# Kernel tuning notes

Hardware: AMD Instinct MI355X
Metric: run time of the kernel (lower is better)

The kernel has to match this reference:

```python
import jax, jax.numpy as jnp
import numpy as np

B, L, E, S, V = 256, 64, 128, 16, 50000
H0, H1 = 16 * E, 4 * E  # dense hidden sizes from dense_sequence_lengths [64,16,4]
PAD_IDX, UNK_IDX = 1, 0


def setup_inputs() -> dict:
    key = jax.random.key(0)
    ks = jax.random.split(key, 12)
    text_lengths = jax.random.randint(ks[0], (B,), 1, L + 1)
    text_lengths = text_lengths.at[0].set(L)  # ensure max(lengths) == L
    raw_tokens = jax.random.randint(ks[1], (B, L), 2, V)
    pos = jnp.arange(L)
    text_batch = jnp.where(pos[None, :] < text_lengths[:, None], raw_tokens, PAD_IDX)
    sentiment_ids = jax.random.randint(ks[2], (B,), 0, 2)

    emb_table = jax.random.normal(ks[3], (V, E), dtype=jnp.float32) * 0.1
    emb_table = emb_table.at[UNK_IDX].set(0.0).at[PAD_IDX].set(0.0)
    sentiment_table = jax.random.normal(ks[4], (2, S), dtype=jnp.float32)
    sentiment_table = sentiment_table / jnp.linalg.norm(sentiment_table, axis=1, keepdims=True)

    D_in = L * E + S + E  # 8336
    W0 = jax.random.normal(ks[5], (D_in, H0), dtype=jnp.float32) * 0.02
    b0 = jax.random.normal(ks[6], (H0,), dtype=jnp.float32) * 0.02
    W1 = jax.random.normal(ks[7], (H0, H1), dtype=jnp.float32) * 0.02
    b1 = jax.random.normal(ks[8], (H1,), dtype=jnp.float32) * 0.02
    Wp = jax.random.normal(ks[9], (H1, 1), dtype=jnp.float32) * 0.02
    bp = jax.random.normal(ks[10], (1,), dtype=jnp.float32) * 0.02
    return {"text_batch": text_batch, "text_lengths": text_lengths,
            "sentiment_ids": sentiment_ids, "emb_table": emb_table,
            "sentiment_table": sentiment_table, "W0": W0, "b0": b0,
            "W1": W1, "b1": b1, "Wp": Wp, "bp": bp}


def reference(text_batch, text_lengths, sentiment_ids, emb_table, sentiment_table,
              W0, b0, W1, b1, Wp, bp):
    # nn.Embedding(max_norm=1.0): renorm rows with norm > 1 (torch uses eps 1e-7)
    norms = jnp.linalg.norm(emb_table, axis=1, keepdims=True)
    w = emb_table * jnp.where(norms > 1.0, 1.0 / (norms + 1e-7), 1.0)
    emb = w[text_batch]                       # (B, L, E)  (dropout is identity in eval)
    sent_flat = emb.reshape(B, L * E)         # flattened sentence embedding
    sv = sentiment_table[sentiment_ids]       # (B, S)

    # First dense layer on concat([sent_flat, sv, word_emb]) factored so the
    # shared sentence/sentiment part is computed once per sentence.
    W_sent, W_snt, W_word = W0[:L * E], W0[L * E:L * E + S], W0[L * E + S:]
    base = sent_flat @ W_sent + sv @ W_snt + b0            # (B, H0)
    h0 = jax.nn.relu(base[:, None, :] + jnp.einsum('ble,eh->blh', emb, W_word))  # (B, L, H0)
    h1 = jax.nn.relu(jnp.einsum('blh,hk->blk', h0, W1) + b1)                      # (B, L, H1)

    # Positions >= text_length keep their zero initialization in encoded_batch
    mask = jnp.arange(L)[None, :] < text_lengths[:, None]  # (B, L)
    enc = jnp.where(mask[:, :, None], h1, 0.0)

    pred = jax.nn.sigmoid(enc @ Wp + bp)[..., 0]           # (B, L)
    return pred
```

## Files before the change

### kernel.cpp

```cpp
#include <hip/hip_runtime.h>
#include <hip/hip_bf16.h>

#define B_   256
#define L_   64
#define E_   128
#define S_   16
#define H0_  2048
#define H1_  512
#define LE_  8192
#define DIN_ 8336
#define NROW 16384

typedef __attribute__((ext_vector_type(8))) short short8_t;
typedef __attribute__((ext_vector_type(4))) float f32x4;

static __device__ __forceinline__ f32x4 mfma16(short8_t a, short8_t b, f32x4 c){
  return __builtin_amdgcn_mfma_f32_16x16x32_bf16(a, b, c, 0, 0, 0);
}

static __device__ __forceinline__ unsigned short f2bf(float x){
  unsigned u = __builtin_bit_cast(unsigned, x);
  unsigned r = u + 0x7FFFu + ((u >> 16) & 1u);
  return (unsigned short)(r >> 16);
}

static __device__ __forceinline__ void gl_lds16(const void* g, void* l){
  __builtin_amdgcn_global_load_lds((const __attribute__((address_space(1))) unsigned*)g,
                                   (__attribute__((address_space(3))) unsigned*)l, 16, 0, 0);
}

__global__ __launch_bounds__(256) void k_scan(const int* __restrict__ lens,
    int* __restrict__ rowmap, int* __restrict__ offs, int* __restrict__ meta){
  __shared__ int sh[256];
  int t = threadIdx.x;
  int v = lens[t];
  sh[t] = v;
  __syncthreads();
  for (int d = 1; d < 256; d <<= 1){
    int y = (t >= d) ? sh[t - d] : 0;
    __syncthreads();
    sh[t] += y;
    __syncthreads();
  }
  int off = sh[t] - v;
  int nv = sh[255];
  offs[t] = off;
  if (t == 0){
    meta[0] = nv;
    meta[1] = (nv + 63) & ~63;
    meta[2] = (nv + 127) & ~127;
  }
  for (int l = 0; l < v; ++l) rowmap[off + l] = t * 64 + l;
  for (int i = nv + t; i < NROW; i += 256) rowmap[i] = 0;
}

__global__ __launch_bounds__(256) void k_transpose_cvt(const float* __restrict__ src,
    unsigned short* __restrict__ dst, int R, int C){
  __shared__ unsigned short tile[64][65];
  int R0 = blockIdx.x * 64, C0 = blockIdx.y * 64;
  int t = threadIdx.x;
  int row = t >> 2, c16 = (t & 3) * 16;
  int gr = R0 + row;
  if (gr < R){
    const float* p = src + (size_t)gr * C + C0 + c16;
    #pragma unroll
    for (int j = 0; j < 16; j += 4){
      float4 v = *reinterpret_cast<const float4*>(p + j);
      tile[row][c16+j+0] = f2bf(v.x);
      tile[row][c16+j+1] = f2bf(v.y);
      tile[row][c16+j+2] = f2bf(v.z);
      tile[row][c16+j+3] = f2bf(v.w);
    }
  }
  __syncthreads();
  int orow = t >> 2, r16 = (t & 3) * 16;
  unsigned short buf[16];
  #pragma unroll
  for (int j = 0; j < 16; ++j) buf[j] = tile[r16 + j][orow];
  unsigned short* q = dst + (size_t)(C0 + orow) * R + R0 + r16;
  if (R0 + r16 + 15 < R){
    *reinterpret_cast<short8_t*>(q)     = *reinterpret_cast<short8_t*>(&buf[0]);
    *reinterpret_cast<short8_t*>(q + 8) = *reinterpret_cast<short8_t*>(&buf[8]);
  } else {
    for (int j = 0; j < 16; ++j) if (R0 + r16 + j < R) q[j] = buf[j];
  }
}

__global__ __launch_bounds__(256) void k_gather(const int* __restrict__ tokens,
    const float* __restrict__ emb, unsigned short* __restrict__ ebf){
  int wid  = blockIdx.x * 4 + (threadIdx.x >> 6);
  int lane = threadIdx.x & 63;
  int tok  = tokens[wid];
  const float* row = emb + (size_t)tok * E_;
  float2 v = *reinterpret_cast<const float2*>(row + lane * 2);
  float ss = v.x * v.x + v.y * v.y;
  #pragma unroll
  for (int m = 1; m < 64; m <<= 1) ss += __shfl_xor(ss, m, 64);
  float nrm = sqrtf(ss);
  float scale = (nrm > 1.0f) ? 1.0f / (nrm + 1e-7f) : 1.0f;
  unsigned a = f2bf(v.x * scale), b = f2bf(v.y * scale);
  *reinterpret_cast<unsigned*>(ebf + (size_t)wid * E_ + lane * 2) = a | (b << 16);
}

static __device__ __forceinline__ void stage64(
    const unsigned short* __restrict__ Asrc, size_t strideA, int m0,
    const unsigned short* __restrict__ Bsrc, size_t strideB, int n0,
    int kbA, int kbB, int w, int lane,
    unsigned short* Al, unsigned short* Bl){
  int rsub = lane >> 3;
  int csw  = 8 * ((lane & 7) ^ rsub);
  #pragma unroll
  for (int c = 0; c < 2; ++c){
    int q = w * 2 + c;
    gl_lds16(Asrc + (size_t)(m0 + q*8 + rsub) * strideA + kbA + csw, Al + q * 512);
  }
  #pragma unroll
  for (int c = 0; c < 4; ++c){
    int q = w * 4 + c;
    gl_lds16(Bsrc + (size_t)(n0 + q*8 + rsub) * strideB + kbB + csw, Bl + q * 512);
  }
}

__global__ __launch_bounds__(256, 2) void k_gemmA(const unsigned short* __restrict__ ebf,
    const unsigned short* __restrict__ W0T, float* __restrict__ part){
  __shared__ unsigned short Al[2][64*64];
  __shared__ unsigned short Bl[2][128*64];
  int bid = blockIdx.x;
  int mt = bid & 3, nt = (bid >> 2) & 15, kw = bid >> 6;
  int m0 = mt * 64, n0 = nt * 128, k0 = kw * 2048;
  int t = threadIdx.x, lane = t & 63, w = t >> 6;
  int wm = w >> 1, wn = w & 1;
  int sw = (lane & 7) * 8, hi = (lane >> 4) * 8, fr = lane & 15;
  f32x4 acc[2][4];
  #pragma unroll
  for (int m = 0; m < 2; ++m)
    #pragma unroll
    for (int n = 0; n < 4; ++n) acc[m][n] = (f32x4){0.f,0.f,0.f,0.f};

  stage64(ebf, LE_, m0, W0T, DIN_, n0, k0, k0, w, lane, Al[0], Bl[0]);
  __syncthreads();
  for (int it = 0; it < 32; ++it){
    int cur = it & 1;
    if (it + 1 < 32)
      stage64(ebf, LE_, m0, W0T, DIN_, n0, k0 + (it+1)*64, k0 + (it+1)*64,
              w, lane, Al[cur^1], Bl[cur^1]);
    #pragma unroll
    for (int ks = 0; ks < 2; ++ks){
      int col = (ks*32 + hi) ^ sw;
      short8_t af[2], bfr[4];
      #pragma unroll
      for (int m = 0; m < 2; ++m)
        af[m] = *reinterpret_cast<const short8_t*>(&Al[cur][(wm*32 + m*16 + fr)*64 + col]);
      #pragma unroll
      for (int n = 0; n < 4; ++n)
        bfr[n] = *reinterpret_cast<const short8_t*>(&Bl[cur][(wn*64 + n*16 + fr)*64 + col]);
      #pragma unroll
      for (int m = 0; m < 2; ++m)
        #pragma unroll
        for (int n = 0; n < 4; ++n) acc[m][n] = mfma16(af[m], bfr[n], acc[m][n]);
    }
    __syncthreads();
  }
  float* P = part + (size_t)kw * B_ * H0_;
  #pragma unroll
  for (int m = 0; m < 2; ++m)
    #pragma unroll
    for (int n = 0; n < 4; ++n)
      #pragma unroll
      for (int i = 0; i < 4; ++i){
        int r = m0 + wm*32 + m*16 + (lane >> 4)*4 + i;
        int c = n0 + wn*64 + n*16 + fr;
        P[(size_t)r * H0_ + c] = acc[m][n][i];
      }
}

__global__ __launch_bounds__(256) void k_base(const int* __restrict__ sid,
    const float* __restrict__ stab, const float* __restrict__ W0,
    const float* __restrict__ b0, const float* __restrict__ part,
    float* __restrict__ base){
  int idx = blockIdx.x * 256 + threadIdx.x;
  int b = idx >> 11, h = idx & 2047;
  const float* sv = stab + sid[b] * S_;
  float acc = b0[h];
  #pragma unroll
  for (int s = 0; s < S_; ++s) acc += sv[s] * W0[(size_t)(LE_ + s) * H0_ + h];
  #pragma unroll
  for (int kw = 0; kw < 4; ++kw) acc += part[(size_t)kw * B_ * H0_ + idx];
  base[idx] = acc;
}

__global__ __launch_bounds__(256, 2) void k_h0(const unsigned short* __restrict__ ebf,
    const unsigned short* __restrict__ W0T, const float* __restrict__ base,
    const int* __restrict__ rowmap, const int* __restrict__ meta,
    unsigned short* __restrict__ h0c){
  int m0 = blockIdx.x * 128;
  if (m0 >= meta[2]) return;
  int n0 = blockIdx.y * 128;
  __shared__ char smem[65536];
  unsigned short* Alds = (unsigned short*)smem;
  unsigned short* Blds = (unsigned short*)(smem + 32768);
  int t = threadIdx.x, lane = t & 63, w = t >> 6;
  int wm = w >> 1, wn = w & 1;
  int sw = (lane & 7) * 8, hi = (lane >> 4) * 8, fr = lane & 15;

  {
    int rsub = lane >> 4;
    int bc = lane & 15;
    #pragma unroll
    for (int c = 0; c < 8; ++c){
      int q = w * 8 + c;
      int row7 = (q & 1) * 4 + rsub;
      int csw = 8 * (bc ^ row7);
      int rm = rowmap[m0 + q*4 + rsub];
      gl_lds16(ebf + (size_t)rm * E_ + csw, Alds + q * 512);
    }
    #pragma unroll
    for (int c = 0; c < 8; ++c){
      int q = w * 8 + c;
      int row7 = (q & 1) * 4 + rsub;
      int csw = 8 * (bc ^ row7);
      gl_lds16(W0T + (size_t)(n0 + q*4 + rsub) * DIN_ + (LE_ + S_) + csw, Blds + q * 512);
    }
  }
  __syncthreads();

  f32x4 acc[4][4];
  #pragma unroll
  for (int m = 0; m < 4; ++m)
    #pragma unroll
    for (int n = 0; n < 4; ++n) acc[m][n] = (f32x4){0.f,0.f,0.f,0.f};
  #pragma unroll
  for (int ks = 0; ks < 4; ++ks){
    int col = (ks*32 + hi) ^ sw;
    short8_t af[4], bfr[4];
    #pragma unroll
    for (int m = 0; m < 4; ++m)
      af[m] = *reinterpret_cast<const short8_t*>(&Alds[(wm*64 + m*16 + fr)*128 + col]);
    #pragma unroll
    for (int n = 0; n < 4; ++n)
      bfr[n] = *reinterpret_cast<const short8_t*>(&Blds[(wn*64 + n*16 + fr)*128 + col]);
    #pragma unroll
    for (int m = 0; m < 4; ++m)
      #pragma unroll
      for (int n = 0; n < 4; ++n) acc[m][n] = mfma16(af[m], bfr[n], acc[m][n]);
  }
  __syncthreads();
  unsigned short* Hs = (unsigned short*)smem;
  #pragma unroll
  for (int m = 0; m < 4; ++m)
    #pragma unroll
    for (int i = 0; i < 4; ++i){
      int row_l = wm*64 + m*16 + (lane >> 4)*4 + i;
      int rm = rowmap[m0 + row_l];
      const float* bb = base + (size_t)(rm >> 6) * H0_ + n0;
      #pragma unroll
      for (int n = 0; n < 4; ++n){
        int col_l = wn*64 + n*16 + fr;
        float vv = acc[m][n][i] + bb[col_l];
        Hs[row_l * 136 + col_l] = f2bf(vv > 0.f ? vv : 0.f);
      }
    }
  __syncthreads();
  int row = t >> 1, half = t & 1;
  const unsigned short* hp = Hs + row * 136 + half * 64;
  unsigned short* gp = h0c + (size_t)(m0 + row) * H0_ + n0 + half * 64;
  #pragma unroll
  for (int j = 0; j < 8; ++j)
    *reinterpret_cast<short8_t*>(gp + j * 8) = *reinterpret_cast<const short8_t*>(hp + j * 8);
}

__global__ __launch_bounds__(256, 2) void k_h1(const unsigned short* __restrict__ h0c,
    const unsigned short* __restrict__ W1T, const float* __restrict__ b1,
    const float* __restrict__ Wp, const int* __restrict__ meta,
    float* __restrict__ logitc){
  int m0 = blockIdx.x * 64;
  if (m0 >= meta[1]) return;
  int n0 = blockIdx.y * 128;
  __shared__ unsigned short Al[2][64*64];
  __shared__ unsigned short Bl[2][128*64];
  int t = threadIdx.x, lane = t & 63, w = t >> 6;
  int wm = w >> 1, wn = w & 1;
  int sw = (lane & 7) * 8, hi = (lane >> 4) * 8, fr = lane & 15;
  f32x4 acc[2][4];
  #pragma unroll
  for (int m = 0; m < 2; ++m)
    #pragma unroll
    for (int n = 0; n < 4; ++n) acc[m][n] = (f32x4){0.f,0.f,0.f,0.f};

  stage64(h0c, H0_, m0, W1T, H0_, n0, 0, 0, w, lane, Al[0], Bl[0]);
  __syncthreads();
  for (int it = 0; it < 32; ++it){
    int cur = it & 1;
    if (it + 1 < 32)
      stage64(h0c, H0_, m0, W1T, H0_, n0, (it+1)*64, (it+1)*64, w, lane, Al[cur^1], Bl[cur^1]);
    #pragma unroll
    for (int ks = 0; ks < 2; ++ks){
      int col = (ks*32 + hi) ^ sw;
      short8_t af[2], bfr[4];
      #pragma unroll
      for (int m = 0; m < 2; ++m)
        af[m] = *reinterpret_cast<const short8_t*>(&Al[cur][(wm*32 + m*16 + fr)*64 + col]);
      #pragma unroll
      for (int n = 0; n < 4; ++n)
        bfr[n] = *reinterpret_cast<const short8_t*>(&Bl[cur][(wn*64 + n*16 + fr)*64 + col]);
      #pragma unroll
      for (int m = 0; m < 2; ++m)
        #pragma unroll
        for (int n = 0; n < 4; ++n) acc[m][n] = mfma16(af[m], bfr[n], acc[m][n]);
    }
    __syncthreads();
  }
  float b1v[4], wpv[4];
  #pragma unroll
  for (int n = 0; n < 4; ++n){
    int col = n0 + wn*64 + n*16 + fr;
    b1v[n] = b1[col]; wpv[n] = Wp[col];
  }
  #pragma unroll
  for (int m = 0; m < 2; ++m)
    #pragma unroll
    for (int i = 0; i < 4; ++i){
      float p = 0.f;
      #pragma unroll
      for (int n = 0; n < 4; ++n){
        float h = acc[m][n][i] + b1v[n];
        h = h > 0.f ? h : 0.f;
        p += h * wpv[n];
      }
      p += __shfl_xor(p, 1); p += __shfl_xor(p, 2);
      p += __shfl_xor(p, 4); p += __shfl_xor(p, 8);
      if ((lane & 15) == 0)
        atomicAdd(&logitc[m0 + wm*32 + m*16 + (lane >> 4)*4 + i], p);
    }
}

__global__ __launch_bounds__(256) void k_finish(const int* __restrict__ lens,
    const int* __restrict__ offs, const float* __restrict__ logitc,
    const float* __restrict__ bp, float* __restrict__ out){
  int idx = blockIdx.x * 256 + threadIdx.x;
  int b = idx >> 6, l = idx & 63;
  float x = bp[0];
  if (l < lens[b]) x += logitc[offs[b] + l];
  out[idx] = 1.f / (1.f + expf(-x));
}

extern "C" void kernel_launch(void* const* d_in, const int* in_sizes, int n_in,
                              void* d_out, int out_size, void* d_ws, size_t ws_size,
                              hipStream_t stream){
  const int*   text = (const int*)d_in[0];
  const int*   lens = (const int*)d_in[1];
  const int*   sid  = (const int*)d_in[2];
  const float* emb  = (const float*)d_in[3];
  const float* stab = (const float*)d_in[4];
  const float* W0   = (const float*)d_in[5];
  const float* b0   = (const float*)d_in[6];
  const float* W1   = (const float*)d_in[7];
  const float* b1   = (const float*)d_in[8];
  const float* Wp   = (const float*)d_in[9];
  const float* bp   = (const float*)d_in[10];
  float* out = (float*)d_out;

  char* ws = (char*)d_ws;
  unsigned short* ebf    = (unsigned short*)(ws);
  unsigned short* W0T    = (unsigned short*)(ws + 4194304);
  unsigned short* W1T    = (unsigned short*)(ws + 38338560);
  float*          base   = (float*)(ws + 40435712);
  float*          part   = (float*)(ws + 42532864);
  float*          logitc = (float*)(ws + 50921472);
  int*            rowmap = (int*)(ws + 50987008);
  int*            offs   = (int*)(ws + 51052544);
  int*            meta   = (int*)(ws + 51053568);
  unsigned short* h0c    = (unsigned short*)(ws + 51054592);

  hipMemsetAsync(logitc, 0, NROW * 4, stream);
  hipLaunchKernelGGL(k_scan,      dim3(1),        dim3(256), 0, stream, lens, rowmap, offs, meta);
  hipLaunchKernelGGL(k_gather,    dim3(4096),     dim3(256), 0, stream, text, emb, ebf);
  hipLaunchKernelGGL(k_transpose_cvt, dim3(131, 32), dim3(256), 0, stream, W0, W0T, DIN_, H0_);
  hipLaunchKernelGGL(k_transpose_cvt, dim3(32, 8),   dim3(256), 0, stream, W1, W1T, H0_, H1_);
  hipLaunchKernelGGL(k_gemmA,     dim3(256),      dim3(256), 0, stream, ebf, W0T, part);
  hipLaunchKernelGGL(k_base,      dim3(2048),     dim3(256), 0, stream, sid, stab, W0, b0, part, base);
  hipLaunchKernelGGL(k_h0,        dim3(128, 16),  dim3(256), 0, stream, ebf, W0T, base, rowmap, meta, h0c);
  hipLaunchKernelGGL(k_h1,        dim3(256, 4),   dim3(256), 0, stream, h0c, W1T, b1, Wp, meta, logitc);
  hipLaunchKernelGGL(k_finish,    dim3(64),       dim3(256), 0, stream, lens, offs, logitc, bp, out);
}
```

Before: 250.8 us.

## Parallelize rowmap fill, halve k_h0 LDS, raise occupancy, reorder grids

The serial per-thread rowmap loop in k_scan moves into a new parallel k_rowfill kernel, which also zeroes logitc in place of the memset. k_h0 now stages K in two 64-wide halves to halve its LDS use, writes bf16 outputs directly to global instead of through an LDS transpose, and raises its launch_bounds occupancy hint. k_gemmA and k_h1 get higher occupancy hints, and k_h0/k_h1 use 1D grids with N tiles varying fastest for better weight reuse in cache. The aim is to cut the serial scan work and improve occupancy, at the cost of an extra kernel launch, an extra barrier in k_h0, and narrower uncoalesced 2-byte global stores.

```diff
diff --git a/kernel.cpp b/kernel.cpp
--- a/kernel.cpp
+++ b/kernel.cpp
@@ -30,7 +30,7 @@
 }
 
 __global__ __launch_bounds__(256) void k_scan(const int* __restrict__ lens,
-    int* __restrict__ rowmap, int* __restrict__ offs, int* __restrict__ meta){
+    int* __restrict__ offs, int* __restrict__ meta){
   __shared__ int sh[256];
   int t = threadIdx.x;
   int v = lens[t];
@@ -50,8 +50,16 @@
     meta[1] = (nv + 63) & ~63;
     meta[2] = (nv + 127) & ~127;
   }
-  for (int l = 0; l < v; ++l) rowmap[off + l] = t * 64 + l;
-  for (int i = nv + t; i < NROW; i += 256) rowmap[i] = 0;
+}
+
+__global__ __launch_bounds__(256) void k_rowfill(const int* __restrict__ lens,
+    const int* __restrict__ offs, const int* __restrict__ meta,
+    int* __restrict__ rowmap, float* __restrict__ logitc){
+  int idx = blockIdx.x * 256 + threadIdx.x;
+  int b = idx >> 6, l = idx & 63;
+  logitc[idx] = 0.f;
+  if (l < lens[b]) rowmap[offs[b] + l] = idx;
+  if (idx >= meta[0]) rowmap[idx] = 0;
 }
 
 __global__ __launch_bounds__(256) void k_transpose_cvt(const float* __restrict__ src,
@@ -121,7 +129,7 @@
   }
 }
 
-__global__ __launch_bounds__(256, 2) void k_gemmA(const unsigned short* __restrict__ ebf,
+__global__ __launch_bounds__(256, 3) void k_gemmA(const unsigned short* __restrict__ ebf,
     const unsigned short* __restrict__ W0T, float* __restrict__ part){
   __shared__ unsigned short Al[2][64*64];
   __shared__ unsigned short Bl[2][128*64];
@@ -189,63 +197,63 @@
   base[idx] = acc;
 }
 
-__global__ __launch_bounds__(256, 2) void k_h0(const unsigned short* __restrict__ ebf,
+__global__ __launch_bounds__(256, 4) void k_h0(const unsigned short* __restrict__ ebf,
     const unsigned short* __restrict__ W0T, const float* __restrict__ base,
     const int* __restrict__ rowmap, const int* __restrict__ meta,
     unsigned short* __restrict__ h0c){
-  int m0 = blockIdx.x * 128;
+  int bid = blockIdx.x;
+  int n0 = (bid & 15) * 128;
+  int m0 = (bid >> 4) * 128;
   if (m0 >= meta[2]) return;
-  int n0 = blockIdx.y * 128;
-  __shared__ char smem[65536];
-  unsigned short* Alds = (unsigned short*)smem;
-  unsigned short* Blds = (unsigned short*)(smem + 32768);
+  __shared__ unsigned short Alds[128*64];
+  __shared__ unsigned short Blds[128*64];
   int t = threadIdx.x, lane = t & 63, w = t >> 6;
   int wm = w >> 1, wn = w & 1;
   int sw = (lane & 7) * 8, hi = (lane >> 4) * 8, fr = lane & 15;
-
-  {
-    int rsub = lane >> 4;
-    int bc = lane & 15;
-    #pragma unroll
-    for (int c = 0; c < 8; ++c){
-      int q = w * 8 + c;
-      int row7 = (q & 1) * 4 + rsub;
-      int csw = 8 * (bc ^ row7);
-      int rm = rowmap[m0 + q*4 + rsub];
-      gl_lds16(ebf + (size_t)rm * E_ + csw, Alds + q * 512);
-    }
-    #pragma unroll
-    for (int c = 0; c < 8; ++c){
-      int q = w * 8 + c;
-      int row7 = (q & 1) * 4 + rsub;
-      int csw = 8 * (bc ^ row7);
-      gl_lds16(W0T + (size_t)(n0 + q*4 + rsub) * DIN_ + (LE_ + S_) + csw, Blds + q * 512);
-    }
-  }
-  __syncthreads();
+  int rsub = lane >> 3;
+  int csw = 8 * ((lane & 7) ^ rsub);
+
+  int rmv[4];
+  #pragma unroll
+  for (int c = 0; c < 4; ++c) rmv[c] = rowmap[m0 + (w*4 + c)*8 + rsub];
 
   f32x4 acc[4][4];
   #pragma unroll
   for (int m = 0; m < 4; ++m)
     #pragma unroll
     for (int n = 0; n < 4; ++n) acc[m][n] = (f32x4){0.f,0.f,0.f,0.f};
-  #pragma unroll
-  for (int ks = 0; ks < 4; ++ks){
-    int col = (ks*32 + hi) ^ sw;
-    short8_t af[4], bfr[4];
-    #pragma unroll
-    for (int m = 0; m < 4; ++m)
-      af[m] = *reinterpret_cast<const short8_t*>(&Alds[(wm*64 + m*16 + fr)*128 + col]);
-    #pragma unroll
-    for (int n = 0; n < 4; ++n)
-      bfr[n] = *reinterpret_cast<const short8_t*>(&Blds[(wn*64 + n*16 + fr)*128 + col]);
-    #pragma unroll
-    for (int m = 0; m < 4; ++m)
-      #pragma unroll
-      for (int n = 0; n < 4; ++n) acc[m][n] = mfma16(af[m], bfr[n], acc[m][n]);
-  }
-  __syncthreads();
-  unsigned short* Hs = (unsigned short*)smem;
+
+  for (int kh = 0; kh < 2; ++kh){
+    if (kh) __syncthreads();
+    int kb = kh * 64;
+    #pragma unroll
+    for (int c = 0; c < 4; ++c){
+      int q = w * 4 + c;
+      gl_lds16(ebf + (size_t)rmv[c] * E_ + kb + csw, Alds + q * 512);
+    }
+    #pragma unroll
+    for (int c = 0; c < 4; ++c){
+      int q = w * 4 + c;
+      gl_lds16(W0T + (size_t)(n0 + q*8 + rsub) * DIN_ + (LE_ + S_) + kb + csw,
+               Blds + q * 512);
+    }
+    __syncthreads();
+    #pragma unroll
+    for (int ks = 0; ks < 2; ++ks){
+      int col = (ks*32 + hi) ^ sw;
+      short8_t af[4], bfr[4];
+      #pragma unroll
+      for (int m = 0; m < 4; ++m)
+        af[m] = *reinterpret_cast<const short8_t*>(&Alds[(wm*64 + m*16 + fr)*64 + col]);
+      #pragma unroll
+      for (int n = 0; n < 4; ++n)
+        bfr[n] = *reinterpret_cast<const short8_t*>(&Blds[(wn*64 + n*16 + fr)*64 + col]);
+      #pragma unroll
+      for (int m = 0; m < 4; ++m)
+        #pragma unroll
+        for (int n = 0; n < 4; ++n) acc[m][n] = mfma16(af[m], bfr[n], acc[m][n]);
+    }
+  }
   #pragma unroll
   for (int m = 0; m < 4; ++m)
     #pragma unroll
@@ -253,29 +261,24 @@
       int row_l = wm*64 + m*16 + (lane >> 4)*4 + i;
       int rm = rowmap[m0 + row_l];
       const float* bb = base + (size_t)(rm >> 6) * H0_ + n0;
+      unsigned short* gp = h0c + (size_t)(m0 + row_l) * H0_ + n0;
       #pragma unroll
       for (int n = 0; n < 4; ++n){
         int col_l = wn*64 + n*16 + fr;
         float vv = acc[m][n][i] + bb[col_l];
-        Hs[row_l * 136 + col_l] = f2bf(vv > 0.f ? vv : 0.f);
+        gp[col_l] = f2bf(vv > 0.f ? vv : 0.f);
       }
     }
-  __syncthreads();
-  int row = t >> 1, half = t & 1;
-  const unsigned short* hp = Hs + row * 136 + half * 64;
-  unsigned short* gp = h0c + (size_t)(m0 + row) * H0_ + n0 + half * 64;
-  #pragma unroll
-  for (int j = 0; j < 8; ++j)
-    *reinterpret_cast<short8_t*>(gp + j * 8) = *reinterpret_cast<const short8_t*>(hp + j * 8);
-}
-
-__global__ __launch_bounds__(256, 2) void k_h1(const unsigned short* __restrict__ h0c,
+}
+
+__global__ __launch_bounds__(256, 3) void k_h1(const unsigned short* __restrict__ h0c,
     const unsigned short* __restrict__ W1T, const float* __restrict__ b1,
     const float* __restrict__ Wp, const int* __restrict__ meta,
     float* __restrict__ logitc){
-  int m0 = blockIdx.x * 64;
+  int bid = blockIdx.x;
+  int n0 = (bid & 3) * 128;
+  int m0 = (bid >> 2) * 64;
   if (m0 >= meta[1]) return;
-  int n0 = blockIdx.y * 128;
   __shared__ unsigned short Al[2][64*64];
   __shared__ unsigned short Bl[2][128*64];
   int t = threadIdx.x, lane = t & 63, w = t >> 6;
@@ -372,14 +375,14 @@
   int*            meta   = (int*)(ws + 51053568);
   unsigned short* h0c    = (unsigned short*)(ws + 51054592);
 
-  hipMemsetAsync(logitc, 0, NROW * 4, stream);
-  hipLaunchKernelGGL(k_scan,      dim3(1),        dim3(256), 0, stream, lens, rowmap, offs, meta);
+  hipLaunchKernelGGL(k_scan,      dim3(1),        dim3(256), 0, stream, lens, offs, meta);
+  hipLaunchKernelGGL(k_rowfill,   dim3(64),       dim3(256), 0, stream, lens, offs, meta, rowmap, logitc);
   hipLaunchKernelGGL(k_gather,    dim3(4096),     dim3(256), 0, stream, text, emb, ebf);
   hipLaunchKernelGGL(k_transpose_cvt, dim3(131, 32), dim3(256), 0, stream, W0, W0T, DIN_, H0_);
   hipLaunchKernelGGL(k_transpose_cvt, dim3(32, 8),   dim3(256), 0, stream, W1, W1T, H0_, H1_);
   hipLaunchKernelGGL(k_gemmA,     dim3(256),      dim3(256), 0, stream, ebf, W0T, part);
   hipLaunchKernelGGL(k_base,      dim3(2048),     dim3(256), 0, stream, sid, stab, W0, b0, part, base);
-  hipLaunchKernelGGL(k_h0,        dim3(128, 16),  dim3(256), 0, stream, ebf, W0T, base, rowmap, meta, h0c);
-  hipLaunchKernelGGL(k_h1,        dim3(256, 4),   dim3(256), 0, stream, h0c, W1T, b1, Wp, meta, logitc);
+  hipLaunchKernelGGL(k_h0,        dim3(2048),     dim3(256), 0, stream, ebf, W0T, base, rowmap, meta, h0c);
+  hipLaunchKernelGGL(k_h1,        dim3(1024),     dim3(256), 0, stream, h0c, W1T, b1, Wp, meta, logitc);
   hipLaunchKernelGGL(k_finish,    dim3(64),       dim3(256), 0, stream, lens, offs, logitc, bp, out);
 }
```

Result: faster. 243.4 us (-3.0%).
